# Kernel optimization log

Measured on AMD Instinct MI355X. Metric: run time of the kernel, lower is better.

The kernel has to match this reference:

```python
import jax, jax.numpy as jnp
import numpy as np

HEADS = 8
DIM_HEAD = 32
EPS = 1e-5


def _rel_index(h, w):
    # matches Attention._generate_relative_index (static, computed on host)
    coords = np.stack(np.meshgrid(np.arange(h), np.arange(w), indexing='ij')).reshape(2, -1)
    rel = coords[:, :, None] - coords[:, None, :]  # [2, n, n]
    rel[0] += h - 1
    rel[1] += w - 1
    rel[0] *= 2 * w - 1
    idx = rel.sum(0).reshape(-1)
    # torch.clamp(relative_index, 0, max_index) -- indices are already in range here
    return jnp.asarray(np.clip(idx, 0, (2 * h - 1) * (2 * w - 1) - 1))


def _layernorm(x, g, b):
    m = jnp.mean(x, axis=-1, keepdims=True)
    v = jnp.var(x, axis=-1, keepdims=True)
    return (x - m) * jax.lax.rsqrt(v + EPS) * g + b


def setup_inputs() -> dict:
    key = jax.random.key(0)
    ks = jax.random.split(key, 6)
    B, C, H, W = 64, 384, 16, 16
    inner = HEADS * DIM_HEAD  # 256
    hid = 4 * C               # 1536
    def nrm(k, shape, s=0.02):
        return jax.random.normal(k, shape, jnp.float32) * s
    return {
        'x': jax.random.normal(ks[0], (B, C, H, W), jnp.float32),
        'ln1_g': jnp.ones((C,), jnp.float32),
        'ln1_b': jnp.zeros((C,), jnp.float32),
        'w_qkv': nrm(ks[1], (C, 3 * inner)),
        'bias_table': nrm(ks[2], ((2 * H - 1) * (2 * W - 1), HEADS)),
        'w_out': nrm(ks[3], (inner, C)),
        'b_out': jnp.zeros((C,), jnp.float32),
        'ln2_g': jnp.ones((C,), jnp.float32),
        'ln2_b': jnp.zeros((C,), jnp.float32),
        'w_ff1': nrm(ks[4], (C, hid)),
        'b_ff1': jnp.zeros((hid,), jnp.float32),
        'w_ff2': nrm(ks[5], (hid, C)),
        'b_ff2': jnp.zeros((C,), jnp.float32),
    }


def reference(x, ln1_g, ln1_b, w_qkv, bias_table, w_out, b_out,
              ln2_g, ln2_b, w_ff1, b_ff1, w_ff2, b_ff2):
    B, C, H, W = x.shape
    n = H * W
    t = x.reshape(B, C, n).transpose(0, 2, 1)  # [B, n, C]

    # --- attention branch (PreNorm(LayerNorm) -> Attention) ---
    a = _layernorm(t, ln1_g, ln1_b)
    qkv = a @ w_qkv  # [B, n, 3*inner]
    q, k, v = jnp.split(qkv, 3, axis=-1)
    def split_heads(z):
        return z.reshape(B, n, HEADS, DIM_HEAD).transpose(0, 2, 1, 3)  # [B, h, n, d]
    q, k, v = split_heads(q), split_heads(k), split_heads(v)
    dots = jnp.einsum('bhid,bhjd->bhij', q, k) * (DIM_HEAD ** -0.5)
    idx = _rel_index(H, W)  # [n*n]
    rel_bias = bias_table[idx].reshape(n, n, HEADS).transpose(2, 0, 1)[None]  # [1, h, n, n]
    attn = jax.nn.softmax(dots + rel_bias, axis=-1)
    o = jnp.einsum('bhij,bhjd->bhid', attn, v)
    o = o.transpose(0, 2, 1, 3).reshape(B, n, HEADS * DIM_HEAD)
    attn_out = o @ w_out + b_out  # to_out Linear (dropout=0)

    # --- feedforward branch (PreNorm(LayerNorm) -> FFN) ---
    f = _layernorm(t, ln2_g, ln2_b)
    f = jax.nn.gelu(f @ w_ff1 + b_ff1, approximate=False) @ w_ff2 + b_ff2

    y = t + attn_out + f  # x_adjusted + attn_out + ff_out
    return y.transpose(0, 2, 1).reshape(B, C, H, W)
```

## Files before the change

### kernel.cpp

```cpp
#include <hip/hip_runtime.h>

typedef __bf16 bf16;
typedef __bf16 bf16x8 __attribute__((ext_vector_type(8)));
typedef float f32x4 __attribute__((ext_vector_type(4)));

__device__ __forceinline__ void gll16(const void* g, void* l) {
    __builtin_amdgcn_global_load_lds((const __attribute__((address_space(1))) void*)g,
                                     (__attribute__((address_space(3))) void*)l, 16, 0, 0);
}

#define WBAR(N) asm volatile("s_waitcnt vmcnt(" #N ")\n\ts_barrier" ::: "memory")

__device__ __forceinline__ float gelu_f(float v) {
    float x2 = v * v;
    float sn = v * fmaf(-0.0713540072f, x2, -1.5957691216f);
    float e  = __expf(sn);
    return v * __builtin_amdgcn_rcpf(1.0f + e);
}

__launch_bounds__(256)
__global__ void prep_kernel(const float* __restrict__ wqkv, const float* __restrict__ wout,
                            const float* __restrict__ wff1, const float* __restrict__ wff2,
                            bf16* __restrict__ wqkvT, bf16* __restrict__ woutT,
                            bf16* __restrict__ wff1T, bf16* __restrict__ wff2T,
                            const float* __restrict__ x,
                            const float* __restrict__ g1, const float* __restrict__ b1,
                            const float* __restrict__ g2, const float* __restrict__ b2,
                            bf16* __restrict__ a, bf16* __restrict__ f) {
    __shared__ __align__(16) float smem[12672 + 512 + 64];
    const int tid = threadIdx.x;
    int g = blockIdx.x;
    if (g < 1536) {
        float (*tl)[33] = (float (*)[33])smem;
        const float* in; bf16* out; int R, Cc, bx, by;
        if (g < 288)       { in = wqkv; out = wqkvT; R = 384;  Cc = 768;  bx = g % 24; by = g / 24; }
        else if (g < 384)  { g -= 288; in = wout; out = woutT; R = 256;  Cc = 384;  bx = g % 12; by = g / 12; }
        else if (g < 960)  { g -= 384; in = wff1; out = wff1T; R = 384;  Cc = 1536; bx = g % 48; by = g / 48; }
        else               { g -= 960; in = wff2; out = wff2T; R = 1536; Cc = 384;  bx = g % 12; by = g / 12; }
        const int c0 = bx * 32, r0 = by * 32;
        const int cl = tid & 31, r8 = tid >> 5;
#pragma unroll
        for (int k = 0; k < 4; k++) {
            int r = k * 8 + r8;
            tl[r][cl] = in[(size_t)(r0 + r) * Cc + c0 + cl];
        }
        __syncthreads();
#pragma unroll
        for (int k = 0; k < 4; k++) {
            int cc = k * 8 + r8;
            out[(size_t)(c0 + cc) * R + r0 + cl] = (bf16)tl[cl][cc];
        }
        return;
    }
    g -= 1536;
    float (*tile)[33] = (float (*)[33])smem;
    float (*S)[32]  = (float (*)[32])(smem + 12672);
    float (*SS)[32] = (float (*)[32])(smem + 12928);
    float* Mn = smem + 13184;
    float* Rs = smem + 13216;
    const int bb = g >> 3;
    const int i0 = (g & 7) * 32;
    {
        const int i_l = tid & 31, c_l = tid >> 5;
        const size_t base = (size_t)bb * 384 * 256 + i0 + i_l;
#pragma unroll 6
        for (int c = c_l; c < 384; c += 8)
            tile[c][i_l] = x[base + (size_t)c * 256];
    }
    __syncthreads();
    {
        const int i_s = tid & 31, p = tid >> 5;
        float s = 0.f, ss = 0.f;
#pragma unroll 6
        for (int j = 0; j < 48; j++) {
            float v = tile[p * 48 + j][i_s];
            s += v; ss += v * v;
        }
        S[p][i_s] = s; SS[p][i_s] = ss;
    }
    __syncthreads();
    if (tid < 32) {
        float t1 = 0.f, t2 = 0.f;
#pragma unroll
        for (int p = 0; p < 8; p++) { t1 += S[p][tid]; t2 += SS[p][tid]; }
        float mean = t1 * (1.0f / 384.0f);
        float var  = t2 * (1.0f / 384.0f) - mean * mean;
        Mn[tid] = mean;
        Rs[tid] = rsqrtf(var + 1e-5f);
    }
    __syncthreads();
    const int lane = tid & 63, w = tid >> 6;
#pragma unroll
    for (int rr = 0; rr < 8; rr++) {
        const int i = w * 8 + rr;
        const float mean = Mn[i], rstd = Rs[i];
        const size_t orow = ((size_t)bb * 256 + i0 + i) * 384;
#pragma unroll
        for (int pass = 0; pass < 6; pass++) {
            const int c = pass * 64 + lane;
            float nh = (tile[c][i] - mean) * rstd;
            a[orow + c] = (bf16)(nh * g1[c] + b1[c]);
            f[orow + c] = (bf16)(nh * g2[c] + b2[c]);
        }
    }
}

#define STAGE128(buf, kb)                                                   \
    {                                                                       \
        bf16* sA = lds + (buf) * 8192;                                      \
        bf16* sB = sA + 4096;                                               \
        gll16(Abase + (size_t)r0 * K + (kb) + k0c, sA + c0 * 8);            \
        gll16(Abase + (size_t)r1 * K + (kb) + k1c, sA + c1 * 8);            \
        gll16(Bbase + (size_t)r0 * K + (kb) + k0c, sB + c0 * 8);            \
        gll16(Bbase + (size_t)r1 * K + (kb) + k1c, sB + c1 * 8);            \
    }
#define COMPUTE128(buf)                                                     \
    {                                                                       \
        const bf16* sA = lds + (buf) * 8192;                                \
        const bf16* sB = sA + 4096;                                         \
        bf16x8 af[4], bfr[4];                                               \
        _Pragma("unroll") for (int i = 0; i < 4; i++)                       \
            af[i] = *(const bf16x8*)(sA + (wm + i * 16 + l16) * 32 + quad * 8); \
        _Pragma("unroll") for (int j = 0; j < 4; j++)                       \
            bfr[j] = *(const bf16x8*)(sB + (wn + j * 16 + l16) * 32 + quad * 8); \
        _Pragma("unroll") for (int i = 0; i < 4; i++)                       \
            _Pragma("unroll") for (int j = 0; j < 4; j++)                   \
                acc[i][j] = __builtin_amdgcn_mfma_f32_16x16x32_bf16(af[i], bfr[j], acc[i][j], 0, 0, 0); \
    }
#define GEMM128_PRO_KLOOP                                                            \
    const int tid = threadIdx.x;                                                     \
    const int g = blockIdx.x;                                                        \
    const int x_ = (g >> 3) % nx;                                                    \
    const int y_ = (g & 7) + 8 * (g / (8 * nx));                                     \
    const int m0 = y_ * 128, n0 = x_ * 128;                                          \
    const int lane = tid & 63, w = tid >> 6;                                         \
    const int l16 = lane & 15, quad = lane >> 4;                                     \
    const int wm = (w & 1) * 64, wn = (w >> 1) * 64;                                 \
    f32x4 zero = {0.f, 0.f, 0.f, 0.f};                                               \
    f32x4 acc[4][4];                                                                 \
    _Pragma("unroll") for (int i = 0; i < 4; i++)                                    \
        _Pragma("unroll") for (int j = 0; j < 4; j++) acc[i][j] = zero;              \
    const int c0 = tid, c1 = tid + 256;                                              \
    const int r0 = c0 >> 2, k0c = (c0 & 3) * 8;                                      \
    const int r1 = c1 >> 2, k1c = (c1 & 3) * 8;                                      \
    const bf16* Abase = A + (size_t)m0 * K;                                          \
    const bf16* Bbase = Bt + (size_t)n0 * K;                                         \
    STAGE128(0, 0);                                                                  \
    STAGE128(1, 32);                                                                 \
    const int nt = K >> 5;                                                           \
    int t = 0;                                                                       \
    for (; t < nt - 2; ++t) {                                                        \
        WBAR(4);                                                                     \
        STAGE128((t + 2) % 3, (t + 2) * 32);                                         \
        COMPUTE128(t % 3);                                                           \
    }                                                                                \
    WBAR(4); COMPUTE128(t % 3); ++t;                                                 \
    WBAR(0); COMPUTE128(t % 3);                                                      \
    __syncthreads();

template <int EPI>
__launch_bounds__(256)
__global__ void gemm_bt(const bf16* __restrict__ A, const bf16* __restrict__ Bt,
                        const float* __restrict__ bias, bf16* __restrict__ C,
                        int M, int N, int K, int nx) {
    __shared__ __align__(16) bf16 lds[24576];
    GEMM128_PRO_KLOOP
#pragma unroll
    for (int j = 0; j < 4; j++) {
        const int col = wn + j * 16 + l16;
        float bv = 0.f;
        if (EPI >= 1) bv = bias[n0 + col];
#pragma unroll
        for (int i = 0; i < 4; i++) {
            const int row0 = wm + i * 16 + quad * 4;
#pragma unroll
            for (int r = 0; r < 4; r++) {
                float v = acc[i][j][r] + bv;
                if (EPI == 2) v = gelu_f(v);
                lds[(row0 + r) * 128 + col] = (bf16)v;
            }
        }
    }
    __syncthreads();
#pragma unroll
    for (int it = 0; it < 8; it++) {
        const int ch = tid + it * 256;
        const int row = ch >> 4, cc = (ch & 15) * 8;
        *(bf16x8*)(C + (size_t)(m0 + row) * N + n0 + cc) = *(const bf16x8*)(lds + row * 128 + cc);
    }
}

__launch_bounds__(256)
__global__ void gemm_bt_tr128(const bf16* __restrict__ A, const bf16* __restrict__ Bt,
                              const float* __restrict__ bias, bf16* __restrict__ Ct,
                              int M, int N, int K, int nx) {
    __shared__ __align__(16) bf16 lds[24576];
    GEMM128_PRO_KLOOP
#pragma unroll
    for (int j = 0; j < 4; j++) {
        const int col = wn + j * 16 + l16;
        const float bv = bias[n0 + col];
#pragma unroll
        for (int i = 0; i < 4; i++) {
            const int row0 = wm + i * 16 + quad * 4;
#pragma unroll
            for (int r = 0; r < 4; r++)
                lds[col * 132 + row0 + r] = (bf16)(acc[i][j][r] + bv);
        }
    }
    __syncthreads();
    const int b = m0 >> 8, ib = m0 & 255;
#pragma unroll
    for (int it = 0; it < 8; it++) {
        const int ch = tid + it * 256;
        const int cl = ch >> 4, ic = (ch & 15) * 8;
        *(bf16x8*)(Ct + ((size_t)(b * 384 + n0 + cl) * 256 + ib + ic)) =
            *(const bf16x8*)(lds + cl * 132 + ic);
    }
}

__launch_bounds__(256)
__global__ void gemm_bt_fin128(const bf16* __restrict__ A, const bf16* __restrict__ Bt,
                               const float* __restrict__ bias,
                               const float* __restrict__ xres, const bf16* __restrict__ attn_t,
                               float* __restrict__ out, int M, int N, int K, int nx) {
    __shared__ __align__(16) bf16 lds[24576];
    GEMM128_PRO_KLOOP
#pragma unroll
    for (int j = 0; j < 4; j++) {
        const int col = wn + j * 16 + l16;
        const float bv = bias[n0 + col];
#pragma unroll
        for (int i = 0; i < 4; i++) {
            const int row0 = wm + i * 16 + quad * 4;
#pragma unroll
            for (int r = 0; r < 4; r++)
                lds[col * 132 + row0 + r] = (bf16)(acc[i][j][r] + bv);
        }
    }
    __syncthreads();
    const int b = m0 >> 8, ib = m0 & 255;
#pragma unroll
    for (int it = 0; it < 8; it++) {
        const int ch = tid + it * 256;
        const int cl = ch >> 4, ic = (ch & 15) * 8;
        const size_t base = (size_t)(b * 384 + n0 + cl) * 256 + ib + ic;
        bf16x8 ff = *(const bf16x8*)(lds + cl * 132 + ic);
        bf16x8 at = *(const bf16x8*)(attn_t + base);
        const f32x4* xr = (const f32x4*)(xres + base);
        f32x4 o0, o1;
#pragma unroll
        for (int e = 0; e < 4; e++) o0[e] = xr[0][e] + (float)at[e] + (float)ff[e];
#pragma unroll
        for (int e = 0; e < 4; e++) o1[e] = xr[1][e] + (float)at[e + 4] + (float)ff[e + 4];
        ((f32x4*)(out + base))[0] = o0;
        ((f32x4*)(out + base))[1] = o1;
    }
}

__launch_bounds__(256)
__global__ void attn_kernel(const bf16* __restrict__ qkv,
                            const float* __restrict__ btab,
                            bf16* __restrict__ o) {
    __shared__ float sbias[961];
    __shared__ __align__(16) bf16 sK[256 * 32];
    __shared__ __align__(16) bf16 sVt[32][264];
    __shared__ __align__(16) bf16 sP[4][16][264];
    const int tid = threadIdx.x;
    const int g = blockIdx.x;
    const int h  = (g >> 3) & 7;
    const int bb = (g & 7) + 8 * (g >> 6);
    const int lane = tid & 63, w = tid >> 6;
    const int l16 = lane & 15, quad = lane >> 4;
    const size_t qkvb = (size_t)bb * 256 * 768;
    const bf16* Qbase = qkv + qkvb + h * 32;
    const bf16* Kbase = qkv + qkvb + 256 + h * 32;
    const bf16* Vbase = qkv + qkvb + 512 + h * 32;

    for (int e = tid; e < 961; e += 256) sbias[e] = btab[e * 8 + h];
#pragma unroll
    for (int it = 0; it < 4; it++) {
        const int ch = it * 256 + tid;
        const int row = ch >> 2, d8 = (ch & 3) * 8;
        gll16(Kbase + (size_t)row * 768 + d8, sK + ch * 8);
    }
#pragma unroll
    for (int it = 0; it < 4; it++) {
        const int ch = it * 256 + tid;
        const int k = ch >> 2, d8 = (ch & 3) * 8;
        bf16x8 vv = *(const bf16x8*)(Vbase + (size_t)k * 768 + d8);
#pragma unroll
        for (int j = 0; j < 8; j++)
            sVt[d8 + j][k] = vv[j];
    }
    __syncthreads();

    f32x4 zero = {0.f, 0.f, 0.f, 0.f};
    for (int qc = 0; qc < 4; qc++) {
        const int qbase = qc * 64 + w * 16;
        bf16x8 qf = *(const bf16x8*)(Qbase + (size_t)(qbase + l16) * 768 + quad * 8);
        f32x4 s[16];
#pragma unroll
        for (int kt = 0; kt < 16; kt++) {
            bf16x8 kf = *(const bf16x8*)(sK + (kt * 16 + l16) * 32 + quad * 8);
            s[kt] = __builtin_amdgcn_mfma_f32_16x16x32_bf16(qf, kf, zero, 0, 0, 0);
        }
        const int qi0 = qbase + quad * 4;
        float mx[4] = {-1e30f, -1e30f, -1e30f, -1e30f};
#pragma unroll
        for (int kt = 0; kt < 16; kt++) {
            const int j = kt * 16 + l16;
            const int yj = j >> 4, xj = j & 15;
#pragma unroll
            for (int r = 0; r < 4; r++) {
                const int q = qi0 + r;
                const int tix = ((q >> 4) - yj + 15) * 31 + ((q & 15) - xj + 15);
                float v = s[kt][r] * 0.17677669529663687f + sbias[tix];
                s[kt][r] = v;
                mx[r] = fmaxf(mx[r], v);
            }
        }
#pragma unroll
        for (int r = 0; r < 4; r++)
            for (int msk = 1; msk < 16; msk <<= 1)
                mx[r] = fmaxf(mx[r], __shfl_xor(mx[r], msk, 64));
        float sum[4] = {0.f, 0.f, 0.f, 0.f};
#pragma unroll
        for (int kt = 0; kt < 16; kt++)
#pragma unroll
            for (int r = 0; r < 4; r++) {
                float e = __expf(s[kt][r] - mx[r]);
                s[kt][r] = e;
                sum[r] += e;
            }
#pragma unroll
        for (int r = 0; r < 4; r++) {
            for (int msk = 1; msk < 16; msk <<= 1)
                sum[r] += __shfl_xor(sum[r], msk, 64);
            sum[r] = 1.0f / sum[r];
        }
#pragma unroll
        for (int kt = 0; kt < 16; kt++)
#pragma unroll
            for (int r = 0; r < 4; r++)
                sP[w][quad * 4 + r][kt * 16 + l16] = (bf16)(s[kt][r] * sum[r]);
        f32x4 oacc[2];
        oacc[0] = zero; oacc[1] = zero;
#pragma unroll
        for (int ks = 0; ks < 8; ks++) {
            bf16x8 pf = *(const bf16x8*)(&sP[w][l16][ks * 32 + quad * 8]);
#pragma unroll
            for (int dt = 0; dt < 2; dt++) {
                bf16x8 vf = *(const bf16x8*)(&sVt[dt * 16 + l16][ks * 32 + quad * 8]);
                oacc[dt] = __builtin_amdgcn_mfma_f32_16x16x32_bf16(pf, vf, oacc[dt], 0, 0, 0);
            }
        }
#pragma unroll
        for (int dt = 0; dt < 2; dt++)
#pragma unroll
            for (int r = 0; r < 4; r++)
                o[(size_t)(bb * 256 + qbase + quad * 4 + r) * 256 + h * 32 + dt * 16 + l16] = (bf16)oacc[dt][r];
    }
}

extern "C" void kernel_launch(void* const* d_in, const int* in_sizes, int n_in,
                              void* d_out, int out_size, void* d_ws, size_t ws_size,
                              hipStream_t stream) {
    const float* x    = (const float*)d_in[0];
    const float* g1   = (const float*)d_in[1];
    const float* b1   = (const float*)d_in[2];
    const float* wqkv = (const float*)d_in[3];
    const float* btab = (const float*)d_in[4];
    const float* wout = (const float*)d_in[5];
    const float* bout = (const float*)d_in[6];
    const float* g2   = (const float*)d_in[7];
    const float* b2   = (const float*)d_in[8];
    const float* wff1 = (const float*)d_in[9];
    const float* bff1 = (const float*)d_in[10];
    const float* wff2 = (const float*)d_in[11];
    const float* bff2 = (const float*)d_in[12];
    float* out = (float*)d_out;

    bf16* ws = (bf16*)d_ws;
    const size_t NA = 6291456;
    bf16* wqkvT = ws;
    bf16* woutT = wqkvT + 294912;
    bf16* wff1T = woutT + 98304;
    bf16* wff2T = wff1T + 589824;
    bf16* f_buf    = ws + 1572864;
    bf16* attn_t   = f_buf + NA;
    bf16* R        = attn_t + NA;
    bf16* a_buf    = R;
    bf16* qkv_buf  = R + NA;
    bf16* o_buf    = R;
    bf16* ffh_buf  = R;

    dim3 b256(256);
    prep_kernel<<<2048, b256, 0, stream>>>(wqkv, wout, wff1, wff2, wqkvT, woutT, wff1T, wff2T,
                                           x, g1, b1, g2, b2, a_buf, f_buf);

    gemm_bt<0><<<6 * 128, b256, 0, stream>>>(a_buf, wqkvT, nullptr, qkv_buf, 16384, 768, 384, 6);
    attn_kernel<<<512, b256, 0, stream>>>(qkv_buf, btab, o_buf);
    gemm_bt_tr128<<<3 * 128, b256, 0, stream>>>(o_buf, woutT, bout, attn_t, 16384, 384, 256, 3);
    gemm_bt<2><<<12 * 128, b256, 0, stream>>>(f_buf, wff1T, bff1, ffh_buf, 16384, 1536, 384, 12);
    gemm_bt_fin128<<<3 * 128, b256, 0, stream>>>(ffh_buf, wff2T, bff2, x, attn_t, out,
                                                 16384, 384, 1536, 3);
}
```

Before: 226.7 us.

## Use 256x256-tile 8-wave pipelined GEMM for QKV and FF1 projections

Adds a new GEMM kernel with 256x256 output tiles, 512 threads and a deeper multi-phase LDS pipeline. It interleaves global-to-LDS staging with 16x16x32 bf16 MFMA bursts under barrier and priority control, and uses a swizzled LDS epilogue for coalesced stores. The QKV and FF1 GEMMs switch from the 128-tile kernel to this one. The aim is more data reuse per tile and better overlap of loads with MFMA work. In exchange the grid has fewer blocks, 128KB of LDS per block and heavy register use, which may hurt occupancy.

```diff
diff --git a/kernel.cpp b/kernel.cpp
--- a/kernel.cpp
+++ b/kernel.cpp
@@ -10,6 +10,8 @@
 }
 
 #define WBAR(N) asm volatile("s_waitcnt vmcnt(" #N ")\n\ts_barrier" ::: "memory")
+#define BARM    asm volatile("s_barrier" ::: "memory")
+#define MFMA16x32 __builtin_amdgcn_mfma_f32_16x16x32_bf16
 
 __device__ __forceinline__ float gelu_f(float v) {
     float x2 = v * v;
@@ -102,6 +104,141 @@
             a[orow + c] = (bf16)(nh * g1[c] + b1[c]);
             f[orow + c] = (bf16)(nh * g2[c] + b2[c]);
         }
+    }
+}
+
+#define RA8(buf, s) ((buf)*65536 + (s)*16384)
+#define RB8(buf, s) ((buf)*65536 + 32768 + (s)*16384)
+#define STHT(rb, bp, kc) (gll16((bp) + srcoff + (kc), lds_b + (rb) + ldst), \
+                          gll16((bp) + srcoff + (kc) + (size_t)128 * K, lds_b + (rb) + ldst + 8192))
+#define NOSTG ((void)0)
+
+#define PHASE8(BUF, S, H, STG, TRAIL)                                               \
+    {                                                                               \
+        const int ab = (BUF)*65536 + (S)*16384 + (wm + (H)*64) * 64 + aoff;         \
+        bf16x8 af0 = *(const bf16x8*)(lds_b + ab);                                  \
+        bf16x8 af1 = *(const bf16x8*)(lds_b + ab + 1024);                           \
+        bf16x8 af2 = *(const bf16x8*)(lds_b + ab + 2048);                           \
+        bf16x8 af3 = *(const bf16x8*)(lds_b + ab + 3072);                           \
+        if ((H) == 0) {                                                             \
+            const int bb2 = (BUF)*65536 + 32768 + (S)*16384 + wn * 64 + aoff;       \
+            bfj0 = *(const bf16x8*)(lds_b + bb2);                                   \
+            bfj1 = *(const bf16x8*)(lds_b + bb2 + 1024);                            \
+            bfj2 = *(const bf16x8*)(lds_b + bb2 + 2048);                            \
+            bfj3 = *(const bf16x8*)(lds_b + bb2 + 3072);                            \
+        }                                                                           \
+        __builtin_amdgcn_sched_barrier(0);                                          \
+        STG;                                                                        \
+        BARM;                                                                       \
+        asm volatile("s_waitcnt lgkmcnt(0)" ::: "memory");                          \
+        __builtin_amdgcn_sched_barrier(0);                                          \
+        __builtin_amdgcn_s_setprio(1);                                              \
+        acc[(H)*4+0][0] = MFMA16x32(af0, bfj0, acc[(H)*4+0][0], 0, 0, 0);           \
+        acc[(H)*4+0][1] = MFMA16x32(af0, bfj1, acc[(H)*4+0][1], 0, 0, 0);           \
+        acc[(H)*4+0][2] = MFMA16x32(af0, bfj2, acc[(H)*4+0][2], 0, 0, 0);           \
+        acc[(H)*4+0][3] = MFMA16x32(af0, bfj3, acc[(H)*4+0][3], 0, 0, 0);           \
+        acc[(H)*4+1][0] = MFMA16x32(af1, bfj0, acc[(H)*4+1][0], 0, 0, 0);           \
+        acc[(H)*4+1][1] = MFMA16x32(af1, bfj1, acc[(H)*4+1][1], 0, 0, 0);           \
+        acc[(H)*4+1][2] = MFMA16x32(af1, bfj2, acc[(H)*4+1][2], 0, 0, 0);           \
+        acc[(H)*4+1][3] = MFMA16x32(af1, bfj3, acc[(H)*4+1][3], 0, 0, 0);           \
+        acc[(H)*4+2][0] = MFMA16x32(af2, bfj0, acc[(H)*4+2][0], 0, 0, 0);           \
+        acc[(H)*4+2][1] = MFMA16x32(af2, bfj1, acc[(H)*4+2][1], 0, 0, 0);           \
+        acc[(H)*4+2][2] = MFMA16x32(af2, bfj2, acc[(H)*4+2][2], 0, 0, 0);           \
+        acc[(H)*4+2][3] = MFMA16x32(af2, bfj3, acc[(H)*4+2][3], 0, 0, 0);           \
+        acc[(H)*4+3][0] = MFMA16x32(af3, bfj0, acc[(H)*4+3][0], 0, 0, 0);           \
+        acc[(H)*4+3][1] = MFMA16x32(af3, bfj1, acc[(H)*4+3][1], 0, 0, 0);           \
+        acc[(H)*4+3][2] = MFMA16x32(af3, bfj2, acc[(H)*4+3][2], 0, 0, 0);           \
+        acc[(H)*4+3][3] = MFMA16x32(af3, bfj3, acc[(H)*4+3][3], 0, 0, 0);           \
+        __builtin_amdgcn_s_setprio(0);                                              \
+        TRAIL;                                                                      \
+    }
+
+template <int EPI>
+__launch_bounds__(512, 2)
+__global__ void gemm8p(const bf16* __restrict__ A, const bf16* __restrict__ Bt,
+                       const float* __restrict__ bias, bf16* __restrict__ C,
+                       int M, int N, int K, int nx) {
+    __shared__ __align__(16) bf16 lds[65536];
+    char* lds_b = (char*)lds;
+    const int tid = threadIdx.x;
+    const int g = blockIdx.x;
+    const int x_ = (g >> 3) % nx;
+    const int y_ = (g & 7) + 8 * (g / (8 * nx));
+    const int m0 = y_ * 256, n0 = x_ * 256;
+    const int lane = tid & 63, w = tid >> 6;
+    const int l16 = lane & 15, quad = lane >> 4;
+    const int wm = (w >> 2) * 128, wn = (w & 3) * 64;
+    const int aoff = l16 * 64 + ((quad ^ ((l16 >> 1) & 3)) * 16);
+    const size_t srcoff = (size_t)(tid >> 2) * K + (size_t)(((tid & 3) ^ ((tid >> 3) & 3)) * 8);
+    const int ldst = tid * 16;
+    const bf16* Abase = A + (size_t)m0 * K;
+    const bf16* Bbase = Bt + (size_t)n0 * K;
+
+    f32x4 acc[8][4];
+    f32x4 zero = {0.f, 0.f, 0.f, 0.f};
+#pragma unroll
+    for (int i = 0; i < 8; i++)
+#pragma unroll
+        for (int j = 0; j < 4; j++) acc[i][j] = zero;
+    bf16x8 bfj0, bfj1, bfj2, bfj3;
+
+    STHT(RA8(0, 0), Abase, 0);
+    STHT(RB8(0, 0), Bbase, 0);
+    STHT(RA8(0, 1), Abase, 32);
+    STHT(RB8(0, 1), Bbase, 32);
+    STHT(RA8(1, 0), Abase, 64);
+    STHT(RB8(1, 0), Bbase, 64);
+    STHT(RA8(1, 1), Abase, 96);
+    WBAR(6);
+
+    const int ng = K >> 7;
+    for (int gq = 0; gq < ng - 1; ++gq) {
+        const int kc = gq * 128;
+        PHASE8(0, 0, 0, STHT(RB8(1, 1), Bbase, kc + 96),  BARM);
+        PHASE8(0, 0, 1, STHT(RA8(0, 0), Abase, kc + 128), BARM);
+        PHASE8(0, 1, 0, STHT(RB8(0, 0), Bbase, kc + 128), BARM);
+        PHASE8(0, 1, 1, STHT(RA8(0, 1), Abase, kc + 160), WBAR(6));
+        PHASE8(1, 0, 0, STHT(RB8(0, 1), Bbase, kc + 160), BARM);
+        PHASE8(1, 0, 1, STHT(RA8(1, 0), Abase, kc + 192), BARM);
+        PHASE8(1, 1, 0, STHT(RB8(1, 0), Bbase, kc + 192), BARM);
+        PHASE8(1, 1, 1, STHT(RA8(1, 1), Abase, kc + 224), WBAR(6));
+    }
+    {
+        const int kc = (ng - 1) * 128;
+        PHASE8(0, 0, 0, STHT(RB8(1, 1), Bbase, kc + 96), BARM);
+        PHASE8(0, 0, 1, NOSTG, BARM);
+        PHASE8(0, 1, 0, NOSTG, BARM);
+        PHASE8(0, 1, 1, NOSTG, WBAR(0));
+        PHASE8(1, 0, 0, NOSTG, BARM);
+        PHASE8(1, 0, 1, NOSTG, BARM);
+        PHASE8(1, 1, 0, NOSTG, BARM);
+        PHASE8(1, 1, 1, NOSTG, BARM);
+    }
+
+#pragma unroll
+    for (int m = 0; m < 8; m++) {
+        const int row = wm + m * 16 + quad * 4;
+#pragma unroll
+        for (int j = 0; j < 4; j++) {
+            const int col = wn + j * 16 + l16;
+            float bv = 0.f;
+            if (EPI >= 1) bv = bias[n0 + col];
+#pragma unroll
+            for (int r = 0; r < 4; r++) {
+                float v = acc[m][j][r] + bv;
+                if (EPI == 2) v = gelu_f(v);
+                const int rr = row + r;
+                *(bf16*)(lds_b + rr * 512 + ((col * 2) ^ ((rr & 7) << 4))) = (bf16)v;
+            }
+        }
+    }
+    __syncthreads();
+#pragma unroll
+    for (int it = 0; it < 16; it++) {
+        const int ch = tid + it * 512;
+        const int row = ch >> 5, c = ch & 31;
+        bf16x8 v = *(const bf16x8*)(lds_b + row * 512 + ((c ^ (row & 7)) * 16));
+        *(bf16x8*)(C + (size_t)(m0 + row) * N + n0 + c * 8) = v;
     }
 }
 
@@ -396,13 +533,14 @@
     bf16* ffh_buf  = R;
 
     dim3 b256(256);
+    dim3 b512(512);
     prep_kernel<<<2048, b256, 0, stream>>>(wqkv, wout, wff1, wff2, wqkvT, woutT, wff1T, wff2T,
                                            x, g1, b1, g2, b2, a_buf, f_buf);
 
-    gemm_bt<0><<<6 * 128, b256, 0, stream>>>(a_buf, wqkvT, nullptr, qkv_buf, 16384, 768, 384, 6);
+    gemm8p<0><<<64 * 3, b512, 0, stream>>>(a_buf, wqkvT, nullptr, qkv_buf, 16384, 768, 384, 3);
     attn_kernel<<<512, b256, 0, stream>>>(qkv_buf, btab, o_buf);
     gemm_bt_tr128<<<3 * 128, b256, 0, stream>>>(o_buf, woutT, bout, attn_t, 16384, 384, 256, 3);
-    gemm_bt<2><<<12 * 128, b256, 0, stream>>>(f_buf, wff1T, bff1, ffh_buf, 16384, 1536, 384, 12);
+    gemm8p<2><<<64 * 6, b512, 0, stream>>>(f_buf, wff1T, bff1, ffh_buf, 16384, 1536, 384, 6);
     gemm_bt_fin128<<<3 * 128, b256, 0, stream>>>(ffh_buf, wff2T, bff2, x, attn_t, out,
                                                  16384, 384, 1536, 3);
 }
```

New measurement: 240.7 us. 6.2% more time.

## Switch GEMMs to 64x384 tiles spanning full output width

Applied to the files above, without the earlier changes.

Replaces the 128x128 GEMM tiling with 64x384 tiles, where each wave computes a 64x96 slice and the B operand covers 384 columns per block. For the out-projection and final FF2 GEMMs, one block now owns all 384 output channels of 64 rows, which simplifies the transposed epilogue and cuts redundant A loads. The cost is more LDS per block (about 84KB across three stages), launch bounds limited to one block per CU, fewer blocks in the N=384 GEMMs (256), and a masked store in the 1536- and 768-wide epilogue.

```diff
diff --git a/kernel.cpp b/kernel.cpp
--- a/kernel.cpp
+++ b/kernel.cpp
@@ -105,147 +105,145 @@
     }
 }
 
-#define STAGE128(buf, kb)                                                   \
-    {                                                                       \
-        bf16* sA = lds + (buf) * 8192;                                      \
-        bf16* sB = sA + 4096;                                               \
-        gll16(Abase + (size_t)r0 * K + (kb) + k0c, sA + c0 * 8);            \
-        gll16(Abase + (size_t)r1 * K + (kb) + k1c, sA + c1 * 8);            \
-        gll16(Bbase + (size_t)r0 * K + (kb) + k0c, sB + c0 * 8);            \
-        gll16(Bbase + (size_t)r1 * K + (kb) + k1c, sB + c1 * 8);            \
-    }
-#define COMPUTE128(buf)                                                     \
-    {                                                                       \
-        const bf16* sA = lds + (buf) * 8192;                                \
-        const bf16* sB = sA + 4096;                                         \
-        bf16x8 af[4], bfr[4];                                               \
-        _Pragma("unroll") for (int i = 0; i < 4; i++)                       \
-            af[i] = *(const bf16x8*)(sA + (wm + i * 16 + l16) * 32 + quad * 8); \
-        _Pragma("unroll") for (int j = 0; j < 4; j++)                       \
-            bfr[j] = *(const bf16x8*)(sB + (wn + j * 16 + l16) * 32 + quad * 8); \
-        _Pragma("unroll") for (int i = 0; i < 4; i++)                       \
-            _Pragma("unroll") for (int j = 0; j < 4; j++)                   \
+#define STAGE_NT(buf, kb)                                                           \
+    {                                                                               \
+        bf16* sA = lds + (buf) * 14336;                                             \
+        bf16* sB = sA + 2048;                                                       \
+        gll16(Abase + (size_t)rA * K + (kb) + kcA, sA + tid * 8);                   \
+        _Pragma("unroll") for (int cB = 0; cB < 6; cB++)                            \
+            gll16(Bbase + (size_t)(rA + 64 * cB) * K + (kb) + kcA,                  \
+                  sB + tid * 8 + cB * 2048);                                        \
+    }
+#define COMPUTE_NT(buf)                                                             \
+    {                                                                               \
+        const bf16* sA = lds + (buf) * 14336;                                       \
+        const bf16* sB = sA + 2048;                                                 \
+        bf16x8 af[4], bfr[6];                                                       \
+        _Pragma("unroll") for (int i = 0; i < 4; i++)                               \
+            af[i] = *(const bf16x8*)(sA + (i * 16 + l16) * 32 + quad * 8);          \
+        _Pragma("unroll") for (int j = 0; j < 6; j++)                               \
+            bfr[j] = *(const bf16x8*)(sB + (wn + j * 16 + l16) * 32 + quad * 8);    \
+        _Pragma("unroll") for (int i = 0; i < 4; i++)                               \
+            _Pragma("unroll") for (int j = 0; j < 6; j++)                           \
                 acc[i][j] = __builtin_amdgcn_mfma_f32_16x16x32_bf16(af[i], bfr[j], acc[i][j], 0, 0, 0); \
     }
-#define GEMM128_PRO_KLOOP                                                            \
-    const int tid = threadIdx.x;                                                     \
-    const int g = blockIdx.x;                                                        \
-    const int x_ = (g >> 3) % nx;                                                    \
-    const int y_ = (g & 7) + 8 * (g / (8 * nx));                                     \
-    const int m0 = y_ * 128, n0 = x_ * 128;                                          \
-    const int lane = tid & 63, w = tid >> 6;                                         \
-    const int l16 = lane & 15, quad = lane >> 4;                                     \
-    const int wm = (w & 1) * 64, wn = (w >> 1) * 64;                                 \
-    f32x4 zero = {0.f, 0.f, 0.f, 0.f};                                               \
-    f32x4 acc[4][4];                                                                 \
-    _Pragma("unroll") for (int i = 0; i < 4; i++)                                    \
-        _Pragma("unroll") for (int j = 0; j < 4; j++) acc[i][j] = zero;              \
-    const int c0 = tid, c1 = tid + 256;                                              \
-    const int r0 = c0 >> 2, k0c = (c0 & 3) * 8;                                      \
-    const int r1 = c1 >> 2, k1c = (c1 & 3) * 8;                                      \
-    const bf16* Abase = A + (size_t)m0 * K;                                          \
-    const bf16* Bbase = Bt + (size_t)n0 * K;                                         \
-    STAGE128(0, 0);                                                                  \
-    STAGE128(1, 32);                                                                 \
-    const int nt = K >> 5;                                                           \
-    int t = 0;                                                                       \
-    for (; t < nt - 2; ++t) {                                                        \
-        WBAR(4);                                                                     \
-        STAGE128((t + 2) % 3, (t + 2) * 32);                                         \
-        COMPUTE128(t % 3);                                                           \
-    }                                                                                \
-    WBAR(4); COMPUTE128(t % 3); ++t;                                                 \
-    WBAR(0); COMPUTE128(t % 3);                                                      \
+#define GEMMNT_CORE                                                                 \
+    const int tid = threadIdx.x;                                                    \
+    const int g = blockIdx.x;                                                       \
+    const int y_ = g / nx;                                                          \
+    const int x_ = g - y_ * nx;                                                     \
+    const int m0 = y_ * 64, n0 = x_ * 384;                                          \
+    const int lane = tid & 63, w = tid >> 6;                                        \
+    const int l16 = lane & 15, quad = lane >> 4;                                    \
+    const int wn = w * 96;                                                          \
+    f32x4 acc[4][6];                                                                \
+    { f32x4 z = {0.f, 0.f, 0.f, 0.f};                                               \
+      _Pragma("unroll") for (int i = 0; i < 4; i++)                                 \
+      _Pragma("unroll") for (int j = 0; j < 6; j++) acc[i][j] = z; }                \
+    const int rA = tid >> 2, kcA = (tid & 3) * 8;                                   \
+    const bf16* Abase = A + (size_t)m0 * K;                                         \
+    const bf16* Bbase = Bt + (size_t)n0 * K;                                        \
+    STAGE_NT(0, 0); STAGE_NT(1, 32);                                                \
+    const int nt = K >> 5;                                                          \
+    int t = 0;                                                                      \
+    for (; t < nt - 2; ++t) {                                                       \
+        WBAR(7);                                                                    \
+        STAGE_NT((t + 2) % 3, (t + 2) * 32);                                        \
+        COMPUTE_NT(t % 3);                                                          \
+    }                                                                               \
+    WBAR(7); COMPUTE_NT(t % 3); ++t;                                                \
+    WBAR(0); COMPUTE_NT(t % 3);                                                     \
     __syncthreads();
 
 template <int EPI>
-__launch_bounds__(256)
-__global__ void gemm_bt(const bf16* __restrict__ A, const bf16* __restrict__ Bt,
+__launch_bounds__(256, 1)
+__global__ void gemm_nt(const bf16* __restrict__ A, const bf16* __restrict__ Bt,
                         const float* __restrict__ bias, bf16* __restrict__ C,
                         int M, int N, int K, int nx) {
-    __shared__ __align__(16) bf16 lds[24576];
-    GEMM128_PRO_KLOOP
-#pragma unroll
-    for (int j = 0; j < 4; j++) {
+    __shared__ __align__(16) bf16 lds[43008];
+    GEMMNT_CORE
+#pragma unroll
+    for (int j = 0; j < 6; j++) {
         const int col = wn + j * 16 + l16;
         float bv = 0.f;
         if (EPI >= 1) bv = bias[n0 + col];
 #pragma unroll
         for (int i = 0; i < 4; i++) {
-            const int row0 = wm + i * 16 + quad * 4;
+            const int row0 = i * 16 + quad * 4;
 #pragma unroll
             for (int r = 0; r < 4; r++) {
                 float v = acc[i][j][r] + bv;
                 if (EPI == 2) v = gelu_f(v);
-                lds[(row0 + r) * 128 + col] = (bf16)v;
+                lds[(row0 + r) * 512 + col] = (bf16)v;
             }
         }
     }
     __syncthreads();
 #pragma unroll
-    for (int it = 0; it < 8; it++) {
+    for (int it = 0; it < 16; it++) {
         const int ch = tid + it * 256;
-        const int row = ch >> 4, cc = (ch & 15) * 8;
-        *(bf16x8*)(C + (size_t)(m0 + row) * N + n0 + cc) = *(const bf16x8*)(lds + row * 128 + cc);
-    }
-}
-
-__launch_bounds__(256)
-__global__ void gemm_bt_tr128(const bf16* __restrict__ A, const bf16* __restrict__ Bt,
-                              const float* __restrict__ bias, bf16* __restrict__ Ct,
-                              int M, int N, int K, int nx) {
-    __shared__ __align__(16) bf16 lds[24576];
-    GEMM128_PRO_KLOOP
-#pragma unroll
-    for (int j = 0; j < 4; j++) {
+        const int row = ch >> 6, cc = (ch & 63) * 8;
+        if (cc < 384)
+            *(bf16x8*)(C + (size_t)(m0 + row) * N + n0 + cc) = *(const bf16x8*)(lds + row * 512 + cc);
+    }
+}
+
+__launch_bounds__(256, 1)
+__global__ void gemm_nt_tr(const bf16* __restrict__ A, const bf16* __restrict__ Bt,
+                           const float* __restrict__ bias, bf16* __restrict__ Ct,
+                           int M, int N, int K, int nx) {
+    __shared__ __align__(16) bf16 lds[43008];
+    GEMMNT_CORE
+#pragma unroll
+    for (int j = 0; j < 6; j++) {
         const int col = wn + j * 16 + l16;
-        const float bv = bias[n0 + col];
+        const float bv = bias[col];
 #pragma unroll
         for (int i = 0; i < 4; i++) {
-            const int row0 = wm + i * 16 + quad * 4;
+            const int row0 = i * 16 + quad * 4;
 #pragma unroll
             for (int r = 0; r < 4; r++)
-                lds[col * 132 + row0 + r] = (bf16)(acc[i][j][r] + bv);
+                lds[col * 72 + row0 + r] = (bf16)(acc[i][j][r] + bv);
         }
     }
     __syncthreads();
     const int b = m0 >> 8, ib = m0 & 255;
 #pragma unroll
-    for (int it = 0; it < 8; it++) {
+    for (int it = 0; it < 12; it++) {
         const int ch = tid + it * 256;
-        const int cl = ch >> 4, ic = (ch & 15) * 8;
-        *(bf16x8*)(Ct + ((size_t)(b * 384 + n0 + cl) * 256 + ib + ic)) =
-            *(const bf16x8*)(lds + cl * 132 + ic);
-    }
-}
-
-__launch_bounds__(256)
-__global__ void gemm_bt_fin128(const bf16* __restrict__ A, const bf16* __restrict__ Bt,
-                               const float* __restrict__ bias,
-                               const float* __restrict__ xres, const bf16* __restrict__ attn_t,
-                               float* __restrict__ out, int M, int N, int K, int nx) {
-    __shared__ __align__(16) bf16 lds[24576];
-    GEMM128_PRO_KLOOP
-#pragma unroll
-    for (int j = 0; j < 4; j++) {
+        const int cl = ch >> 3, ic = (ch & 7) * 8;
+        *(bf16x8*)(Ct + ((size_t)(b * 384 + cl) * 256 + ib + ic)) =
+            *(const bf16x8*)(lds + cl * 72 + ic);
+    }
+}
+
+__launch_bounds__(256, 1)
+__global__ void gemm_nt_fin(const bf16* __restrict__ A, const bf16* __restrict__ Bt,
+                            const float* __restrict__ bias,
+                            const float* __restrict__ xres, const bf16* __restrict__ attn_t,
+                            float* __restrict__ out, int M, int N, int K, int nx) {
+    __shared__ __align__(16) bf16 lds[43008];
+    GEMMNT_CORE
+#pragma unroll
+    for (int j = 0; j < 6; j++) {
         const int col = wn + j * 16 + l16;
-        const float bv = bias[n0 + col];
+        const float bv = bias[col];
 #pragma unroll
         for (int i = 0; i < 4; i++) {
-            const int row0 = wm + i * 16 + quad * 4;
+            const int row0 = i * 16 + quad * 4;
 #pragma unroll
             for (int r = 0; r < 4; r++)
-                lds[col * 132 + row0 + r] = (bf16)(acc[i][j][r] + bv);
+                lds[col * 72 + row0 + r] = (bf16)(acc[i][j][r] + bv);
         }
     }
     __syncthreads();
     const int b = m0 >> 8, ib = m0 & 255;
 #pragma unroll
-    for (int it = 0; it < 8; it++) {
+    for (int it = 0; it < 12; it++) {
         const int ch = tid + it * 256;
-        const int cl = ch >> 4, ic = (ch & 15) * 8;
-        const size_t base = (size_t)(b * 384 + n0 + cl) * 256 + ib + ic;
-        bf16x8 ff = *(const bf16x8*)(lds + cl * 132 + ic);
+        const int cl = ch >> 3, ic = (ch & 7) * 8;
+        const size_t base = (size_t)(b * 384 + cl) * 256 + ib + ic;
+        bf16x8 ff = *(const bf16x8*)(lds + cl * 72 + ic);
         bf16x8 at = *(const bf16x8*)(attn_t + base);
         const f32x4* xr = (const f32x4*)(xres + base);
         f32x4 o0, o1;
@@ -399,10 +397,10 @@
     prep_kernel<<<2048, b256, 0, stream>>>(wqkv, wout, wff1, wff2, wqkvT, woutT, wff1T, wff2T,
                                            x, g1, b1, g2, b2, a_buf, f_buf);
 
-    gemm_bt<0><<<6 * 128, b256, 0, stream>>>(a_buf, wqkvT, nullptr, qkv_buf, 16384, 768, 384, 6);
+    gemm_nt<0><<<256 * 2, b256, 0, stream>>>(a_buf, wqkvT, nullptr, qkv_buf, 16384, 768, 384, 2);
     attn_kernel<<<512, b256, 0, stream>>>(qkv_buf, btab, o_buf);
-    gemm_bt_tr128<<<3 * 128, b256, 0, stream>>>(o_buf, woutT, bout, attn_t, 16384, 384, 256, 3);
-    gemm_bt<2><<<12 * 128, b256, 0, stream>>>(f_buf, wff1T, bff1, ffh_buf, 16384, 1536, 384, 12);
-    gemm_bt_fin128<<<3 * 128, b256, 0, stream>>>(ffh_buf, wff2T, bff2, x, attn_t, out,
-                                                 16384, 384, 1536, 3);
-}
+    gemm_nt_tr<<<256, b256, 0, stream>>>(o_buf, woutT, bout, attn_t, 16384, 384, 256, 1);
+    gemm_nt<2><<<256 * 4, b256, 0, stream>>>(f_buf, wff1T, bff1, ffh_buf, 16384, 1536, 384, 4);
+    gemm_nt_fin<<<256, b256, 0, stream>>>(ffh_buf, wff2T, bff2, x, attn_t, out,
+                                          16384, 384, 1536, 1);
+}
```

After: 253.3 us. +11.7%, slower.

## Load GEMM operands directly into registers instead of staging through LDS

Applied to the files above, without the earlier changes.

Replaces the LDS triple-buffered global_load_lds pipeline in all three 128x128 GEMM kernels with per-wave direct global-to-register loads, double-buffered in two register sets. This removes the per-iteration barriers and LDS traffic, and shrinks the shared allocation so launch bounds can request 3 blocks per SM. In exchange, each wave now fetches its own A/B slices from global memory, so data that was shared across waves through LDS is loaded redundantly and the kernel relies on caches. Register pressure also rises.

```diff
diff --git a/kernel.cpp b/kernel.cpp
--- a/kernel.cpp
+++ b/kernel.cpp
@@ -4,12 +4,12 @@
 typedef __bf16 bf16x8 __attribute__((ext_vector_type(8)));
 typedef float f32x4 __attribute__((ext_vector_type(4)));
 
+#define MFMA16x32 __builtin_amdgcn_mfma_f32_16x16x32_bf16
+
 __device__ __forceinline__ void gll16(const void* g, void* l) {
     __builtin_amdgcn_global_load_lds((const __attribute__((address_space(1))) void*)g,
                                      (__attribute__((address_space(3))) void*)l, 16, 0, 0);
 }
-
-#define WBAR(N) asm volatile("s_waitcnt vmcnt(" #N ")\n\ts_barrier" ::: "memory")
 
 __device__ __forceinline__ float gelu_f(float v) {
     float x2 = v * v;
@@ -105,29 +105,17 @@
     }
 }
 
-#define STAGE128(buf, kb)                                                   \
-    {                                                                       \
-        bf16* sA = lds + (buf) * 8192;                                      \
-        bf16* sB = sA + 4096;                                               \
-        gll16(Abase + (size_t)r0 * K + (kb) + k0c, sA + c0 * 8);            \
-        gll16(Abase + (size_t)r1 * K + (kb) + k1c, sA + c1 * 8);            \
-        gll16(Bbase + (size_t)r0 * K + (kb) + k0c, sB + c0 * 8);            \
-        gll16(Bbase + (size_t)r1 * K + (kb) + k1c, sB + c1 * 8);            \
-    }
-#define COMPUTE128(buf)                                                     \
-    {                                                                       \
-        const bf16* sA = lds + (buf) * 8192;                                \
-        const bf16* sB = sA + 4096;                                         \
-        bf16x8 af[4], bfr[4];                                               \
-        _Pragma("unroll") for (int i = 0; i < 4; i++)                       \
-            af[i] = *(const bf16x8*)(sA + (wm + i * 16 + l16) * 32 + quad * 8); \
-        _Pragma("unroll") for (int j = 0; j < 4; j++)                       \
-            bfr[j] = *(const bf16x8*)(sB + (wn + j * 16 + l16) * 32 + quad * 8); \
-        _Pragma("unroll") for (int i = 0; i < 4; i++)                       \
-            _Pragma("unroll") for (int j = 0; j < 4; j++)                   \
-                acc[i][j] = __builtin_amdgcn_mfma_f32_16x16x32_bf16(af[i], bfr[j], acc[i][j], 0, 0, 0); \
-    }
-#define GEMM128_PRO_KLOOP                                                            \
+#define RLOAD(s, kb)                                                        \
+    { _Pragma("unroll") for (int i = 0; i < 4; i++)                         \
+          s##a[i] = *(const bf16x8*)(pA + (size_t)i * 16 * K + (kb));       \
+      _Pragma("unroll") for (int j = 0; j < 4; j++)                         \
+          s##b[j] = *(const bf16x8*)(pB + (size_t)j * 16 * K + (kb)); }
+#define RMFMA(s)                                                            \
+    { _Pragma("unroll") for (int i = 0; i < 4; i++)                         \
+      _Pragma("unroll") for (int j = 0; j < 4; j++)                         \
+          acc[i][j] = MFMA16x32(s##a[i], s##b[j], acc[i][j], 0, 0, 0); }
+
+#define GEMMR_CORE                                                                   \
     const int tid = threadIdx.x;                                                     \
     const int g = blockIdx.x;                                                        \
     const int x_ = (g >> 3) % nx;                                                    \
@@ -136,35 +124,34 @@
     const int lane = tid & 63, w = tid >> 6;                                         \
     const int l16 = lane & 15, quad = lane >> 4;                                     \
     const int wm = (w & 1) * 64, wn = (w >> 1) * 64;                                 \
-    f32x4 zero = {0.f, 0.f, 0.f, 0.f};                                               \
     f32x4 acc[4][4];                                                                 \
-    _Pragma("unroll") for (int i = 0; i < 4; i++)                                    \
-        _Pragma("unroll") for (int j = 0; j < 4; j++) acc[i][j] = zero;              \
-    const int c0 = tid, c1 = tid + 256;                                              \
-    const int r0 = c0 >> 2, k0c = (c0 & 3) * 8;                                      \
-    const int r1 = c1 >> 2, k1c = (c1 & 3) * 8;                                      \
-    const bf16* Abase = A + (size_t)m0 * K;                                          \
-    const bf16* Bbase = Bt + (size_t)n0 * K;                                         \
-    STAGE128(0, 0);                                                                  \
-    STAGE128(1, 32);                                                                 \
+    { f32x4 z = {0.f, 0.f, 0.f, 0.f};                                                \
+      _Pragma("unroll") for (int i = 0; i < 4; i++)                                  \
+      _Pragma("unroll") for (int j = 0; j < 4; j++) acc[i][j] = z; }                 \
+    const bf16* pA = A + (size_t)(m0 + wm + l16) * K + quad * 8;                     \
+    const bf16* pB = Bt + (size_t)(n0 + wn + l16) * K + quad * 8;                    \
+    bf16x8 Pa[4], Pb[4], Qa[4], Qb[4];                                               \
+    RLOAD(P, 0);                                                                     \
     const int nt = K >> 5;                                                           \
-    int t = 0;                                                                       \
-    for (; t < nt - 2; ++t) {                                                        \
-        WBAR(4);                                                                     \
-        STAGE128((t + 2) % 3, (t + 2) * 32);                                         \
-        COMPUTE128(t % 3);                                                           \
+    int kb = 0;                                                                      \
+    for (int t = 0; t < nt - 2; t += 2) {                                            \
+        RLOAD(Q, kb + 32);                                                           \
+        RMFMA(P);                                                                    \
+        RLOAD(P, kb + 64);                                                           \
+        RMFMA(Q);                                                                    \
+        kb += 64;                                                                    \
     }                                                                                \
-    WBAR(4); COMPUTE128(t % 3); ++t;                                                 \
-    WBAR(0); COMPUTE128(t % 3);                                                      \
-    __syncthreads();
+    RLOAD(Q, kb + 32);                                                               \
+    RMFMA(P);                                                                        \
+    RMFMA(Q);
 
 template <int EPI>
-__launch_bounds__(256)
-__global__ void gemm_bt(const bf16* __restrict__ A, const bf16* __restrict__ Bt,
-                        const float* __restrict__ bias, bf16* __restrict__ C,
-                        int M, int N, int K, int nx) {
-    __shared__ __align__(16) bf16 lds[24576];
-    GEMM128_PRO_KLOOP
+__launch_bounds__(256, 3)
+__global__ void gemm_r(const bf16* __restrict__ A, const bf16* __restrict__ Bt,
+                       const float* __restrict__ bias, bf16* __restrict__ C,
+                       int M, int N, int K, int nx) {
+    __shared__ __align__(16) bf16 lds[16384];
+    GEMMR_CORE
 #pragma unroll
     for (int j = 0; j < 4; j++) {
         const int col = wn + j * 16 + l16;
@@ -190,12 +177,12 @@
     }
 }
 
-__launch_bounds__(256)
-__global__ void gemm_bt_tr128(const bf16* __restrict__ A, const bf16* __restrict__ Bt,
-                              const float* __restrict__ bias, bf16* __restrict__ Ct,
-                              int M, int N, int K, int nx) {
-    __shared__ __align__(16) bf16 lds[24576];
-    GEMM128_PRO_KLOOP
+__launch_bounds__(256, 3)
+__global__ void gemm_r_tr(const bf16* __restrict__ A, const bf16* __restrict__ Bt,
+                          const float* __restrict__ bias, bf16* __restrict__ Ct,
+                          int M, int N, int K, int nx) {
+    __shared__ __align__(16) bf16 lds[16896];
+    GEMMR_CORE
 #pragma unroll
     for (int j = 0; j < 4; j++) {
         const int col = wn + j * 16 + l16;
@@ -219,13 +206,13 @@
     }
 }
 
-__launch_bounds__(256)
-__global__ void gemm_bt_fin128(const bf16* __restrict__ A, const bf16* __restrict__ Bt,
-                               const float* __restrict__ bias,
-                               const float* __restrict__ xres, const bf16* __restrict__ attn_t,
-                               float* __restrict__ out, int M, int N, int K, int nx) {
-    __shared__ __align__(16) bf16 lds[24576];
-    GEMM128_PRO_KLOOP
+__launch_bounds__(256, 3)
+__global__ void gemm_r_fin(const bf16* __restrict__ A, const bf16* __restrict__ Bt,
+                           const float* __restrict__ bias,
+                           const float* __restrict__ xres, const bf16* __restrict__ attn_t,
+                           float* __restrict__ out, int M, int N, int K, int nx) {
+    __shared__ __align__(16) bf16 lds[16896];
+    GEMMR_CORE
 #pragma unroll
     for (int j = 0; j < 4; j++) {
         const int col = wn + j * 16 + l16;
@@ -399,10 +386,10 @@
     prep_kernel<<<2048, b256, 0, stream>>>(wqkv, wout, wff1, wff2, wqkvT, woutT, wff1T, wff2T,
                                            x, g1, b1, g2, b2, a_buf, f_buf);
 
-    gemm_bt<0><<<6 * 128, b256, 0, stream>>>(a_buf, wqkvT, nullptr, qkv_buf, 16384, 768, 384, 6);
+    gemm_r<0><<<6 * 128, b256, 0, stream>>>(a_buf, wqkvT, nullptr, qkv_buf, 16384, 768, 384, 6);
     attn_kernel<<<512, b256, 0, stream>>>(qkv_buf, btab, o_buf);
-    gemm_bt_tr128<<<3 * 128, b256, 0, stream>>>(o_buf, woutT, bout, attn_t, 16384, 384, 256, 3);
-    gemm_bt<2><<<12 * 128, b256, 0, stream>>>(f_buf, wff1T, bff1, ffh_buf, 16384, 1536, 384, 12);
-    gemm_bt_fin128<<<3 * 128, b256, 0, stream>>>(ffh_buf, wff2T, bff2, x, attn_t, out,
-                                                 16384, 384, 1536, 3);
-}
+    gemm_r_tr<<<3 * 128, b256, 0, stream>>>(o_buf, woutT, bout, attn_t, 16384, 384, 256, 3);
+    gemm_r<2><<<12 * 128, b256, 0, stream>>>(f_buf, wff1T, bff1, ffh_buf, 16384, 1536, 384, 12);
+    gemm_r_fin<<<3 * 128, b256, 0, stream>>>(ffh_buf, wff2T, bff2, x, attn_t, out,
+                                             16384, 384, 1536, 3);
+}
```

Result: slower. 347.6 us (+53.3%).
